# Kernel tuning notes

Measured on AMD Instinct MI355X. Metric: run time of the kernel, lower is better.

## Reference

```python
import jax, jax.numpy as jnp
import numpy as np

EPS = 1e-5

def rmsnorm(x, w):
    return x * jax.lax.rsqrt(jnp.mean(x * x, axis=-1, keepdims=True) + EPS) * w

def setup_inputs() -> dict:
    key = jax.random.key(0)
    ks = jax.random.split(key, 10)
    b, d, n, k, r, l = 64, 256, 16, 4, 16, 256
    inp = {}
    inp['x_1'] = jax.random.normal(ks[0], (b, d), jnp.float32)
    inp['x_2'] = jax.random.normal(ks[1], (b, d), jnp.float32)
    inp['norm_w'] = jnp.ones((d,), jnp.float32)
    inp['conv_w'] = jax.random.normal(ks[2], (d, 1, k), jnp.float32) * 0.2
    inp['conv_b'] = jax.random.normal(ks[3], (d,), jnp.float32) * 0.02
    inp['in_w'] = jax.random.normal(ks[4], (2 * d, d), jnp.float32) * 0.02
    inp['xproj_w'] = jax.random.normal(ks[5], (r + 2 * n, d), jnp.float32) * 0.02
    inp['dt_w'] = jax.random.normal(ks[6], (d, r), jnp.float32) * 0.02
    inp['dt_b'] = jax.random.normal(ks[7], (d,), jnp.float32) * 0.02
    inp['out_w'] = jax.random.normal(ks[8], (d, d), jnp.float32) * 0.02
    # A = repeat(arange(1, n+1), 'n -> d n'); A_log = log(A)
    inp['A_log'] = jnp.tile(jnp.log(jnp.arange(1, n + 1, dtype=jnp.float32)), (d, 1))
    inp['D'] = jnp.ones((d,), jnp.float32)
    inp['l'] = l
    return inp

def _dwconv(x, conv_w, conv_b, l):
    # x: (b, l, d); depthwise causal-ish conv with padding k-1 on both sides, truncate to l
    d = x.shape[-1]
    k = conv_w.shape[-1]
    xt = x.transpose(0, 2, 1)  # (b, d, l)
    out = jax.lax.conv_general_dilated(
        xt, conv_w, window_strides=(1,), padding=[(k - 1, k - 1)],
        dimension_numbers=('NCH', 'OIH', 'NCH'), feature_group_count=d)
    out = out[:, :, :l] + conv_b[None, :, None]
    return out.transpose(0, 2, 1)  # (b, l, d)

def reference(x_1, x_2, norm_w, conv_w, conv_b, in_w, xproj_w, dt_w, dt_b, out_w, A_log, D, l):
    b, d = x_1.shape
    n = A_log.shape[1]
    r = dt_w.shape[1]
    # RMSNorm then broadcast along sequence
    x1 = jnp.broadcast_to(rmsnorm(x_1, norm_w)[:, None, :], (b, l, d))
    x2 = jnp.broadcast_to(rmsnorm(x_2, norm_w)[:, None, :], (b, l, d))
    # in_proj (no bias), split into x and res
    xr1 = x1 @ in_w.T
    x1c, res1 = xr1[..., :d], xr1[..., d:]
    xr2 = x2 @ in_w.T
    x2c, _ = xr2[..., :d], xr2[..., d:]
    # depthwise conv + silu
    x1s = jax.nn.silu(_dwconv(x1c, conv_w, conv_b, l))
    x2s = jax.nn.silu(_dwconv(x2c, conv_w, conv_b, l))
    # ssm: delta/B/C from x2s, scanned input u = x1s
    A = -jnp.exp(A_log)  # (d, n)
    xdbl = x2s @ xproj_w.T  # (b, l, r + 2n)
    delta, B, C = xdbl[..., :r], xdbl[..., r:r + n], xdbl[..., r + n:]
    delta = jax.nn.softplus(delta @ dt_w.T + dt_b)  # (b, l, d)
    deltaA = jnp.exp(jnp.einsum('bld,dn->bldn', delta, A))  # (b, l, d, n)
    dBu = (delta * x1s)[..., None] * B[:, :, None, :]  # (b, l, d, n)
    def step(h, inputs):
        dA_i, dBu_i, C_i = inputs  # (b,d,n), (b,d,n), (b,n)
        h = dA_i * h + dBu_i
        y = jnp.einsum('bdn,bn->bd', h, C_i)
        return h, y
    h0 = jnp.zeros((b, d, n), x1s.dtype)
    _, ys = jax.lax.scan(step, h0, (deltaA.transpose(1, 0, 2, 3),
                                     dBu.transpose(1, 0, 2, 3),
                                     C.transpose(1, 0, 2)))
    y = ys.transpose(1, 0, 2) + x1s * D  # (b, l, d)
    y = y * jax.nn.silu(res1)
    out = rmsnorm(y @ out_w.T, norm_w)
    return out[:, -1, :]
```

## Files before the change

### kernel.cpp

```cpp
#include <hip/hip_runtime.h>
#include <math.h>

#define D 256
#define N 16
#define R 16

__device__ __forceinline__ float silu_f(float x) {
    return x / (1.0f + expf(-x));
}

__device__ __forceinline__ float softplus_f(float x) {
    return fmaxf(x, 0.0f) + log1pf(expf(-fabsf(x)));
}

__device__ __forceinline__ float block_reduce_sum(float v, float* s_red) {
    #pragma unroll
    for (int off = 32; off >= 1; off >>= 1)
        v += __shfl_down(v, off, 64);
    const int wave = threadIdx.x >> 6;
    const int lane = threadIdx.x & 63;
    __syncthreads();
    if (lane == 0) s_red[wave] = v;
    __syncthreads();
    return s_red[0] + s_red[1] + s_red[2] + s_red[3];
}

__global__ __launch_bounds__(256) void mamba_collapsed_kernel(
    const float* __restrict__ x1_in, const float* __restrict__ x2_in,
    const float* __restrict__ norm_w, const float* __restrict__ conv_w,
    const float* __restrict__ conv_b, const float* __restrict__ in_w,
    const float* __restrict__ xproj_w, const float* __restrict__ dt_w,
    const float* __restrict__ dt_b, const float* __restrict__ out_w,
    const float* __restrict__ A_log, const float* __restrict__ Dp,
    const int* __restrict__ l_ptr, float* __restrict__ out)
{
    const int b = blockIdx.x;
    const int j = threadIdx.x;
    const int l = *l_ptr;

    __shared__ float s_n1[D];
    __shared__ float s_n2[D];
    __shared__ float s_x2s[4][D];
    __shared__ float s_xdbl[4][48];
    __shared__ float s_y[D];
    __shared__ float s_red[4];

    const float v1 = x1_in[b * D + j];
    const float v2 = x2_in[b * D + j];
    const float ss1 = block_reduce_sum(v1 * v1, s_red);
    const float ss2 = block_reduce_sum(v2 * v2, s_red);
    const float wn = norm_w[j];
    s_n1[j] = v1 * rsqrtf(ss1 * (1.0f / D) + 1e-5f) * wn;
    s_n2[j] = v2 * rsqrtf(ss2 * (1.0f / D) + 1e-5f) * wn;
    __syncthreads();

    const float* __restrict__ wrow_a = in_w + (size_t)j * D;
    const float* __restrict__ wrow_b = in_w + (size_t)(j + D) * D;
    float x1c = 0.0f, res1 = 0.0f, x2c = 0.0f;
    #pragma unroll 4
    for (int i = 0; i < D; i += 4) {
        const float4 wa = *(const float4*)(wrow_a + i);
        const float4 wb = *(const float4*)(wrow_b + i);
        const float n1x = s_n1[i], n1y = s_n1[i+1], n1z = s_n1[i+2], n1w = s_n1[i+3];
        const float n2x = s_n2[i], n2y = s_n2[i+1], n2z = s_n2[i+2], n2w = s_n2[i+3];
        x1c  += wa.x*n1x + wa.y*n1y + wa.z*n1z + wa.w*n1w;
        res1 += wb.x*n1x + wb.y*n1y + wb.z*n1z + wb.w*n1w;
        x2c  += wa.x*n2x + wa.y*n2y + wa.z*n2z + wa.w*n2w;
    }

    const float cw0 = conv_w[j*4 + 0], cw1 = conv_w[j*4 + 1],
                cw2 = conv_w[j*4 + 2], cw3 = conv_w[j*4 + 3];
    const float cb = conv_b[j];
    float ksum[4];
    ksum[0] = cw3;
    ksum[1] = cw2 + cw3;
    ksum[2] = cw1 + cw2 + cw3;
    ksum[3] = cw0 + cw1 + cw2 + cw3;
    float x1s[4];
    #pragma unroll
    for (int tc = 0; tc < 4; ++tc) {
        x1s[tc] = silu_f(ksum[tc] * x1c + cb);
        s_x2s[tc][j] = silu_f(ksum[tc] * x2c + cb);
    }
    __syncthreads();

    if (j < 192) {
        const int tc = j / 48;
        const int o  = j % 48;
        const float* __restrict__ prow = xproj_w + (size_t)o * D;
        const float* __restrict__ xs   = s_x2s[tc];
        float acc = 0.0f;
        #pragma unroll 4
        for (int i = 0; i < D; i += 4) {
            const float4 p = *(const float4*)(prow + i);
            acc += p.x*xs[i] + p.y*xs[i+1] + p.z*xs[i+2] + p.w*xs[i+3];
        }
        s_xdbl[tc][o] = acc;
    }
    __syncthreads();

    const float* __restrict__ dtrow = dt_w + (size_t)j * R;
    float dtr[R];
    #pragma unroll
    for (int q = 0; q < R; ++q) dtr[q] = dtrow[q];
    const float dtb = dt_b[j];
    float delta[4];
    #pragma unroll
    for (int tc = 0; tc < 4; ++tc) {
        float acc = 0.0f;
        #pragma unroll
        for (int q = 0; q < R; ++q) acc += s_xdbl[tc][q] * dtr[q];
        delta[tc] = softplus_f(acc + dtb);
    }

    const float* __restrict__ arow = A_log + (size_t)j * N;
    float Aa[N];
    #pragma unroll
    for (int n = 0; n < N; ++n) Aa[n] = -expf(arow[n]);

    float h[N];
    #pragma unroll
    for (int n = 0; n < N; ++n) h[n] = 0.0f;

    const int nexp = (l < 3) ? l : 3;
    for (int t = 0; t < nexp; ++t) {
        const float dl = delta[t];
        const float du = dl * x1s[t];
        #pragma unroll
        for (int n = 0; n < N; ++n) {
            const float dA = expf(dl * Aa[n]);
            h[n] = dA * h[n] + du * s_xdbl[t][16 + n];
        }
    }
    if (l > 3) {
        const float dl = delta[3];
        const float du = dl * x1s[3];
        const float steps = (float)(l - 3);
        #pragma unroll
        for (int n = 0; n < N; ++n) {
            const float z   = dl * Aa[n];
            const float em1 = expm1f(z);
            const float emN = expm1f(steps * z);
            const float ratio = (em1 != 0.0f) ? (emN / em1) : steps;
            const float p = emN + 1.0f;
            h[n] = p * h[n] + du * s_xdbl[3][16 + n] * ratio;
        }
    }

    const int fc = ((l - 1) < 3) ? (l - 1) : 3;
    float y = 0.0f;
    #pragma unroll
    for (int n = 0; n < N; ++n) y += h[n] * s_xdbl[fc][32 + n];
    y += x1s[fc] * Dp[j];
    y *= silu_f(res1);
    s_y[j] = y;
    __syncthreads();

    const float* __restrict__ orow = out_w + (size_t)j * D;
    float z = 0.0f;
    #pragma unroll 4
    for (int i = 0; i < D; i += 4) {
        const float4 ow = *(const float4*)(orow + i);
        z += ow.x*s_y[i] + ow.y*s_y[i+1] + ow.z*s_y[i+2] + ow.w*s_y[i+3];
    }
    const float ssz = block_reduce_sum(z * z, s_red);
    out[b * D + j] = z * rsqrtf(ssz * (1.0f / D) + 1e-5f) * norm_w[j];
}

extern "C" void kernel_launch(void* const* d_in, const int* in_sizes, int n_in,
                              void* d_out, int out_size, void* d_ws, size_t ws_size,
                              hipStream_t stream) {
    const float* x1      = (const float*)d_in[0];
    const float* x2      = (const float*)d_in[1];
    const float* norm_w  = (const float*)d_in[2];
    const float* conv_w  = (const float*)d_in[3];
    const float* conv_b  = (const float*)d_in[4];
    const float* in_w    = (const float*)d_in[5];
    const float* xproj_w = (const float*)d_in[6];
    const float* dt_w    = (const float*)d_in[7];
    const float* dt_b    = (const float*)d_in[8];
    const float* out_w   = (const float*)d_in[9];
    const float* A_log   = (const float*)d_in[10];
    const float* Dp      = (const float*)d_in[11];
    const int*   l_ptr   = (const int*)d_in[12];
    float* out = (float*)d_out;

    const int batch = in_sizes[0] / D;
    mamba_collapsed_kernel<<<dim3(batch), dim3(D), 0, stream>>>(
        x1, x2, norm_w, conv_w, conv_b, in_w, xproj_w, dt_w, dt_b,
        out_w, A_log, Dp, l_ptr, out);
}
```

Baseline: 114.0 us.

## Split fused kernel into three launches with split-K dot products

```diff
diff --git a/kernel.cpp b/kernel.cpp
--- a/kernel.cpp
+++ b/kernel.cpp
@@ -5,166 +5,212 @@
 #define N 16
 #define R 16
 
-__device__ __forceinline__ float silu_f(float x) {
-    return x / (1.0f + expf(-x));
-}
-
+#define WS_X1C  0
+#define WS_RES1 16384
+#define WS_X2C  32768
+#define WS_Y    49152
+
+__device__ __forceinline__ float silu_f(float x) { return x / (1.0f + expf(-x)); }
 __device__ __forceinline__ float softplus_f(float x) {
     return fmaxf(x, 0.0f) + log1pf(expf(-fabsf(x)));
 }
 
-__device__ __forceinline__ float block_reduce_sum(float v, float* s_red) {
-    #pragma unroll
-    for (int off = 32; off >= 1; off >>= 1)
-        v += __shfl_down(v, off, 64);
-    const int wave = threadIdx.x >> 6;
-    const int lane = threadIdx.x & 63;
-    __syncthreads();
-    if (lane == 0) s_red[wave] = v;
-    __syncthreads();
-    return s_red[0] + s_red[1] + s_red[2] + s_red[3];
-}
-
-__global__ __launch_bounds__(256) void mamba_collapsed_kernel(
+__global__ __launch_bounds__(256) void k_inw(
     const float* __restrict__ x1_in, const float* __restrict__ x2_in,
-    const float* __restrict__ norm_w, const float* __restrict__ conv_w,
-    const float* __restrict__ conv_b, const float* __restrict__ in_w,
+    const float* __restrict__ norm_w, const float* __restrict__ in_w,
+    float* __restrict__ ws)
+{
+    __shared__ float s_n[D];
+    __shared__ float s_red[4];
+    const int t  = threadIdx.x;
+    const int g0 = blockIdx.x * 64;
+    const int b  = g0 / 768;
+    const int o0 = g0 % 768;
+    const bool use2 = (o0 >= 512);
+
+    const float* __restrict__ xrow = (use2 ? x2_in : x1_in) + (size_t)b * D;
+    const float v = xrow[t];
+    float p = v * v;
+    #pragma unroll
+    for (int off = 32; off >= 1; off >>= 1) p += __shfl_down(p, off, 64);
+    if ((t & 63) == 0) s_red[t >> 6] = p;
+    __syncthreads();
+    const float ss = s_red[0] + s_red[1] + s_red[2] + s_red[3];
+    s_n[t] = v * rsqrtf(ss * (1.0f / D) + 1e-5f) * norm_w[t];
+    __syncthreads();
+
+    const int o   = o0 + (t >> 2);
+    const int q   = t & 3;
+    const int row = (o >= 512) ? (o - 512) : o;
+    const float* __restrict__ wr = in_w + (size_t)row * D;
+    float acc = 0.0f;
+    #pragma unroll
+    for (int k = 0; k < 16; ++k) {
+        const int e = q * 4 + 16 * k;
+        const float4 w4 = *(const float4*)(wr + e);
+        const float4 n4 = *(const float4*)(s_n + e);
+        acc += w4.x*n4.x + w4.y*n4.y + w4.z*n4.z + w4.w*n4.w;
+    }
+    acc += __shfl_xor(acc, 1, 64);
+    acc += __shfl_xor(acc, 2, 64);
+    if (q == 0) {
+        const int jj = o & 255;
+        float* dst = (o < 256) ? (ws + WS_X1C)
+                   : (o < 512) ? (ws + WS_RES1)
+                               : (ws + WS_X2C);
+        dst[b * D + jj] = acc;
+    }
+}
+
+__global__ __launch_bounds__(1024) void k_scan(
+    const float* __restrict__ conv_w, const float* __restrict__ conv_b,
     const float* __restrict__ xproj_w, const float* __restrict__ dt_w,
-    const float* __restrict__ dt_b, const float* __restrict__ out_w,
-    const float* __restrict__ A_log, const float* __restrict__ Dp,
-    const int* __restrict__ l_ptr, float* __restrict__ out)
+    const float* __restrict__ dt_b, const float* __restrict__ A_log,
+    const float* __restrict__ Dp, const int* __restrict__ l_ptr,
+    float* __restrict__ ws)
 {
-    const int b = blockIdx.x;
-    const int j = threadIdx.x;
-    const int l = *l_ptr;
-
-    __shared__ float s_n1[D];
-    __shared__ float s_n2[D];
     __shared__ float s_x2s[4][D];
     __shared__ float s_xdbl[4][48];
+    const int b = blockIdx.x;
+    const int t = threadIdx.x;
+    const int l = *l_ptr;
+
+    float x1s[4];
+    if (t < D) {
+        const float x1c = ws[WS_X1C + b * D + t];
+        const float x2c = ws[WS_X2C + b * D + t];
+        const float4 cw = *(const float4*)(conv_w + 4 * t);
+        const float cb  = conv_b[t];
+        float ksum[4];
+        ksum[0] = cw.w;
+        ksum[1] = cw.z + cw.w;
+        ksum[2] = cw.y + cw.z + cw.w;
+        ksum[3] = cw.x + cw.y + cw.z + cw.w;
+        #pragma unroll
+        for (int tc = 0; tc < 4; ++tc) {
+            x1s[tc] = silu_f(ksum[tc] * x1c + cb);
+            s_x2s[tc][t] = silu_f(ksum[tc] * x2c + cb);
+        }
+    }
+    __syncthreads();
+
+    if (t < 768) {
+        const int dotid = t >> 2;
+        const int q     = t & 3;
+        const int tc    = dotid / 48;
+        const int o     = dotid % 48;
+        const float* __restrict__ pr = xproj_w + (size_t)o * D;
+        const float* __restrict__ xs = s_x2s[tc];
+        float acc = 0.0f;
+        #pragma unroll
+        for (int k = 0; k < 16; ++k) {
+            const int e = q * 4 + 16 * k;
+            const float4 p4 = *(const float4*)(pr + e);
+            const float4 x4 = *(const float4*)(xs + e);
+            acc += p4.x*x4.x + p4.y*x4.y + p4.z*x4.z + p4.w*x4.w;
+        }
+        acc += __shfl_xor(acc, 1, 64);
+        acc += __shfl_xor(acc, 2, 64);
+        if (q == 0) s_xdbl[tc][o] = acc;
+    }
+    __syncthreads();
+
+    if (t < D) {
+        const int j = t;
+        const float* __restrict__ dtrow = dt_w + (size_t)j * R;
+        float dtr[R];
+        #pragma unroll
+        for (int qq = 0; qq < R; ++qq) dtr[qq] = dtrow[qq];
+        const float dtb = dt_b[j];
+        float delta[4];
+        #pragma unroll
+        for (int tc = 0; tc < 4; ++tc) {
+            float acc = 0.0f;
+            #pragma unroll
+            for (int qq = 0; qq < R; ++qq) acc += s_xdbl[tc][qq] * dtr[qq];
+            delta[tc] = softplus_f(acc + dtb);
+        }
+        const float* __restrict__ arow = A_log + (size_t)j * N;
+        float Aa[N];
+        #pragma unroll
+        for (int n = 0; n < N; ++n) Aa[n] = -expf(arow[n]);
+        float h[N];
+        #pragma unroll
+        for (int n = 0; n < N; ++n) h[n] = 0.0f;
+        const int nexp = (l < 3) ? l : 3;
+        for (int tt = 0; tt < nexp; ++tt) {
+            const float dl = delta[tt];
+            const float du = dl * x1s[tt];
+            #pragma unroll
+            for (int n = 0; n < N; ++n) {
+                const float dA = expf(dl * Aa[n]);
+                h[n] = dA * h[n] + du * s_xdbl[tt][16 + n];
+            }
+        }
+        if (l > 3) {
+            const float dl = delta[3];
+            const float du = dl * x1s[3];
+            const float steps = (float)(l - 3);
+            #pragma unroll
+            for (int n = 0; n < N; ++n) {
+                const float z   = dl * Aa[n];
+                const float em1 = expm1f(z);
+                const float emN = expm1f(steps * z);
+                const float ratio = (em1 != 0.0f) ? (emN / em1) : steps;
+                const float pw = emN + 1.0f;
+                h[n] = pw * h[n] + du * s_xdbl[3][16 + n] * ratio;
+            }
+        }
+        const int fc = ((l - 1) < 3) ? (l - 1) : 3;
+        float y = 0.0f;
+        #pragma unroll
+        for (int n = 0; n < N; ++n) y += h[n] * s_xdbl[fc][32 + n];
+        y += x1s[fc] * Dp[j];
+        const float res1 = ws[WS_RES1 + b * D + j];
+        y *= silu_f(res1);
+        ws[WS_Y + b * D + j] = y;
+    }
+}
+
+__global__ __launch_bounds__(1024) void k_out(
+    const float* __restrict__ ws, const float* __restrict__ out_w,
+    const float* __restrict__ norm_w, float* __restrict__ out)
+{
     __shared__ float s_y[D];
-    __shared__ float s_red[4];
-
-    const float v1 = x1_in[b * D + j];
-    const float v2 = x2_in[b * D + j];
-    const float ss1 = block_reduce_sum(v1 * v1, s_red);
-    const float ss2 = block_reduce_sum(v2 * v2, s_red);
-    const float wn = norm_w[j];
-    s_n1[j] = v1 * rsqrtf(ss1 * (1.0f / D) + 1e-5f) * wn;
-    s_n2[j] = v2 * rsqrtf(ss2 * (1.0f / D) + 1e-5f) * wn;
-    __syncthreads();
-
-    const float* __restrict__ wrow_a = in_w + (size_t)j * D;
-    const float* __restrict__ wrow_b = in_w + (size_t)(j + D) * D;
-    float x1c = 0.0f, res1 = 0.0f, x2c = 0.0f;
-    #pragma unroll 4
-    for (int i = 0; i < D; i += 4) {
-        const float4 wa = *(const float4*)(wrow_a + i);
-        const float4 wb = *(const float4*)(wrow_b + i);
-        const float n1x = s_n1[i], n1y = s_n1[i+1], n1z = s_n1[i+2], n1w = s_n1[i+3];
-        const float n2x = s_n2[i], n2y = s_n2[i+1], n2z = s_n2[i+2], n2w = s_n2[i+3];
-        x1c  += wa.x*n1x + wa.y*n1y + wa.z*n1z + wa.w*n1w;
-        res1 += wb.x*n1x + wb.y*n1y + wb.z*n1z + wb.w*n1w;
-        x2c  += wa.x*n2x + wa.y*n2y + wa.z*n2z + wa.w*n2w;
-    }
-
-    const float cw0 = conv_w[j*4 + 0], cw1 = conv_w[j*4 + 1],
-                cw2 = conv_w[j*4 + 2], cw3 = conv_w[j*4 + 3];
-    const float cb = conv_b[j];
-    float ksum[4];
-    ksum[0] = cw3;
-    ksum[1] = cw2 + cw3;
-    ksum[2] = cw1 + cw2 + cw3;
-    ksum[3] = cw0 + cw1 + cw2 + cw3;
-    float x1s[4];
-    #pragma unroll
-    for (int tc = 0; tc < 4; ++tc) {
-        x1s[tc] = silu_f(ksum[tc] * x1c + cb);
-        s_x2s[tc][j] = silu_f(ksum[tc] * x2c + cb);
-    }
-    __syncthreads();
-
-    if (j < 192) {
-        const int tc = j / 48;
-        const int o  = j % 48;
-        const float* __restrict__ prow = xproj_w + (size_t)o * D;
-        const float* __restrict__ xs   = s_x2s[tc];
-        float acc = 0.0f;
-        #pragma unroll 4
-        for (int i = 0; i < D; i += 4) {
-            const float4 p = *(const float4*)(prow + i);
-            acc += p.x*xs[i] + p.y*xs[i+1] + p.z*xs[i+2] + p.w*xs[i+3];
-        }
-        s_xdbl[tc][o] = acc;
-    }
-    __syncthreads();
-
-    const float* __restrict__ dtrow = dt_w + (size_t)j * R;
-    float dtr[R];
-    #pragma unroll
-    for (int q = 0; q < R; ++q) dtr[q] = dtrow[q];
-    const float dtb = dt_b[j];
-    float delta[4];
-    #pragma unroll
-    for (int tc = 0; tc < 4; ++tc) {
-        float acc = 0.0f;
-        #pragma unroll
-        for (int q = 0; q < R; ++q) acc += s_xdbl[tc][q] * dtr[q];
-        delta[tc] = softplus_f(acc + dtb);
-    }
-
-    const float* __restrict__ arow = A_log + (size_t)j * N;
-    float Aa[N];
-    #pragma unroll
-    for (int n = 0; n < N; ++n) Aa[n] = -expf(arow[n]);
-
-    float h[N];
-    #pragma unroll
-    for (int n = 0; n < N; ++n) h[n] = 0.0f;
-
-    const int nexp = (l < 3) ? l : 3;
-    for (int t = 0; t < nexp; ++t) {
-        const float dl = delta[t];
-        const float du = dl * x1s[t];
-        #pragma unroll
-        for (int n = 0; n < N; ++n) {
-            const float dA = expf(dl * Aa[n]);
-            h[n] = dA * h[n] + du * s_xdbl[t][16 + n];
-        }
-    }
-    if (l > 3) {
-        const float dl = delta[3];
-        const float du = dl * x1s[3];
-        const float steps = (float)(l - 3);
-        #pragma unroll
-        for (int n = 0; n < N; ++n) {
-            const float z   = dl * Aa[n];
-            const float em1 = expm1f(z);
-            const float emN = expm1f(steps * z);
-            const float ratio = (em1 != 0.0f) ? (emN / em1) : steps;
-            const float p = emN + 1.0f;
-            h[n] = p * h[n] + du * s_xdbl[3][16 + n] * ratio;
-        }
-    }
-
-    const int fc = ((l - 1) < 3) ? (l - 1) : 3;
-    float y = 0.0f;
-    #pragma unroll
-    for (int n = 0; n < N; ++n) y += h[n] * s_xdbl[fc][32 + n];
-    y += x1s[fc] * Dp[j];
-    y *= silu_f(res1);
-    s_y[j] = y;
-    __syncthreads();
-
-    const float* __restrict__ orow = out_w + (size_t)j * D;
-    float z = 0.0f;
-    #pragma unroll 4
-    for (int i = 0; i < D; i += 4) {
-        const float4 ow = *(const float4*)(orow + i);
-        z += ow.x*s_y[i] + ow.y*s_y[i+1] + ow.z*s_y[i+2] + ow.w*s_y[i+3];
-    }
-    const float ssz = block_reduce_sum(z * z, s_red);
-    out[b * D + j] = z * rsqrtf(ssz * (1.0f / D) + 1e-5f) * norm_w[j];
+    __shared__ float s_z[D];
+    __shared__ float s_red[16];
+    const int b = blockIdx.x;
+    const int t = threadIdx.x;
+
+    if (t < D) s_y[t] = ws[WS_Y + b * D + t];
+    __syncthreads();
+
+    const int o = t >> 2;
+    const int q = t & 3;
+    const float* __restrict__ orow = out_w + (size_t)o * D;
+    float acc = 0.0f;
+    #pragma unroll
+    for (int k = 0; k < 16; ++k) {
+        const int e = q * 4 + 16 * k;
+        const float4 w4 = *(const float4*)(orow + e);
+        const float4 y4 = *(const float4*)(s_y + e);
+        acc += w4.x*y4.x + w4.y*y4.y + w4.z*y4.z + w4.w*y4.w;
+    }
+    acc += __shfl_xor(acc, 1, 64);
+    acc += __shfl_xor(acc, 2, 64);
+    if (q == 0) s_z[o] = acc;
+    __syncthreads();
+
+    const float zz = (t < D) ? s_z[t] : 0.0f;
+    float p = zz * zz;
+    #pragma unroll
+    for (int off = 32; off >= 1; off >>= 1) p += __shfl_down(p, off, 64);
+    if ((t & 63) == 0) s_red[t >> 6] = p;
+    __syncthreads();
+    if (t < D) {
+        const float ss = s_red[0] + s_red[1] + s_red[2] + s_red[3];
+        out[b * D + t] = zz * rsqrtf(ss * (1.0f / D) + 1e-5f) * norm_w[t];
+    }
 }
 
 extern "C" void kernel_launch(void* const* d_in, const int* in_sizes, int n_in,
@@ -184,9 +230,12 @@
     const float* Dp      = (const float*)d_in[11];
     const int*   l_ptr   = (const int*)d_in[12];
     float* out = (float*)d_out;
+    float* ws  = (float*)d_ws;
 
     const int batch = in_sizes[0] / D;
-    mamba_collapsed_kernel<<<dim3(batch), dim3(D), 0, stream>>>(
-        x1, x2, norm_w, conv_w, conv_b, in_w, xproj_w, dt_w, dt_b,
-        out_w, A_log, Dp, l_ptr, out);
-}
+
+    k_inw<<<dim3(batch * 12), dim3(256), 0, stream>>>(x1, x2, norm_w, in_w, ws);
+    k_scan<<<dim3(batch), dim3(1024), 0, stream>>>(conv_w, conv_b, xproj_w,
+                                                   dt_w, dt_b, A_log, Dp, l_ptr, ws);
+    k_out<<<dim3(batch), dim3(1024), 0, stream>>>(ws, out_w, norm_w, out);
+}
```

Measured after the change: 96.95 us. 15.0% less time.
